# Performance work log

Hardware: AMD Instinct MI355X
Metric: run time of the kernel (lower is better)

The kernel has to match this reference:

```python
import jax, jax.numpy as jnp
import numpy as np

N_NODES = 1_000_000
N_EDGES = 8_000_000
EMB = 64
CHANNELS = 2
C_DIM = EMB // CHANNELS
NEG_SLOPE = 0.01  # nn.LeakyReLU default
EPS = 1e-10


def setup_inputs() -> dict:
    key = jax.random.key(0)
    k1, k2, k3, k4, k5 = jax.random.split(key, 5)
    ego_emb = jax.random.normal(k1, (N_NODES, EMB), dtype=jnp.float32)
    W = jax.random.normal(k2, (CHANNELS, EMB, C_DIM), dtype=jnp.float32) * (1.0 / np.sqrt(EMB))
    b = jax.random.normal(k3, (CHANNELS, 1, C_DIM), dtype=jnp.float32) * 0.01
    row_indices = jax.random.randint(k4, (N_EDGES,), 0, N_NODES, dtype=jnp.int32)
    col_indices = jax.random.randint(k5, (N_EDGES,), 0, N_NODES, dtype=jnp.int32)
    return {"ego_emb": ego_emb, "W": W, "b": b,
            "row_indices": row_indices, "col_indices": col_indices}


def _channel_gat(ego_emb, Wc, bc, row, col, n_nodes):
    # project nodes to this disentangled channel: [N, c_dim]
    h = jax.nn.leaky_relu(ego_emb @ Wc + bc, NEG_SLOPE)
    h_row = h[row]                      # [E, c_dim] edge gather (dst)
    h_col = h[col]                      # [E, c_dim] edge gather (src)
    logits = jax.nn.leaky_relu(jnp.sum(h_row * h_col, axis=-1), NEG_SLOPE)  # [E]
    # edge softmax per destination row (numerically stable)
    row_max = jax.ops.segment_max(logits, row, num_segments=n_nodes)
    ex = jnp.exp(logits - row_max[row])
    denom = jax.ops.segment_sum(ex, row, num_segments=n_nodes)
    alpha = ex / (denom[row] + EPS)     # [E]
    # scatter-add weighted messages into destination rows
    return jax.ops.segment_sum(alpha[:, None] * h_col, row, num_segments=n_nodes)


def reference(ego_emb, W, b, row_indices, col_indices):
    outs = [
        _channel_gat(ego_emb, W[c], b[c], row_indices, col_indices, ego_emb.shape[0])
        for c in range(CHANNELS)
    ]
    return jnp.concatenate(outs, axis=-1)  # [N, emb_size]
```

## Files before the change

kernel.cpp:

```cpp
#include <hip/hip_runtime.h>
#include <stdint.h>

#define NEG_SLOPE 0.01f
#define EPSF 1e-10f
#define NB_SHIFT 11
#define NB_ROWS (1 << NB_SHIFT)
#define NB_MAX 512
#define BP_EPT 16
#define BP_EDGES (256 * BP_EPT)
#define CB_CAP 20480

__device__ __forceinline__ float lrelu(float x){
  return fmaxf(x, 0.f) + NEG_SLOPE * fminf(x, 0.f);
}

__global__ void conv_wb(const float* __restrict__ W,
                        const float* __restrict__ b,
                        float* __restrict__ Wf, float* __restrict__ bf){
  int i = blockIdx.x * blockDim.x + threadIdx.x;
  for (int idx = i; idx < 64 * 64; idx += blockDim.x * gridDim.x){
    int k = idx >> 6, j = idx & 63;
    int c = j >> 5, jj = j & 31;
    Wf[idx] = W[c * 2048 + k * 32 + jj];
  }
  if (i < 64) bf[i] = b[i];
}

__global__ __launch_bounds__(256) void proj(const float* __restrict__ ego,
                                            const float* __restrict__ Wf,
                                            const float* __restrict__ bf,
                                            float* __restrict__ h, int N){
  int n = blockIdx.x * 256 + threadIdx.x;
  if (n >= N) return;
  float acc[64];
  #pragma unroll
  for (int j = 0; j < 64; j++) acc[j] = bf[j];
  const float4* ep = (const float4*)(ego + (size_t)n * 64);
  for (int kk = 0; kk < 16; kk++){
    float4 q = ep[kk];
    float ev[4] = {q.x, q.y, q.z, q.w};
    const float* wbase = Wf + kk * 4 * 64;
    #pragma unroll
    for (int t = 0; t < 4; t++){
      float ek = ev[t];
      const float* wrow = wbase + t * 64;
      #pragma unroll
      for (int j = 0; j < 64; j++) acc[j] = fmaf(ek, wrow[j], acc[j]);
    }
  }
  float4* hp = (float4*)(h + (size_t)n * 64);
  #pragma unroll
  for (int v = 0; v < 16; v++){
    float4 o;
    o.x = lrelu(acc[4 * v + 0]);
    o.y = lrelu(acc[4 * v + 1]);
    o.z = lrelu(acc[4 * v + 2]);
    o.w = lrelu(acc[4 * v + 3]);
    hp[v] = o;
  }
}

__global__ __launch_bounds__(256) void bhist(const int* __restrict__ row,
                                             int* __restrict__ bcnt, int E, int nb){
  __shared__ int lh[NB_MAX];
  for (int i = threadIdx.x; i < nb; i += 256) lh[i] = 0;
  __syncthreads();
  int i = blockIdx.x * 256 + threadIdx.x;
  int stride = gridDim.x * 256;
  for (; i < E; i += stride) atomicAdd(&lh[row[i] >> NB_SHIFT], 1);
  __syncthreads();
  for (int j = threadIdx.x; j < nb; j += 256){
    int v = lh[j];
    if (v) atomicAdd(&bcnt[j], v);
  }
}

__global__ __launch_bounds__(512) void bscan(const int* __restrict__ bcnt,
                                             int* __restrict__ bbase,
                                             int* __restrict__ bcur, int nb){
  __shared__ int sh[NB_MAX];
  int t = threadIdx.x;
  int v = (t < nb) ? bcnt[t] : 0;
  sh[t] = v; __syncthreads();
  for (int off = 1; off < NB_MAX; off <<= 1){
    int a = (t >= off) ? sh[t - off] : 0;
    __syncthreads();
    sh[t] += a;
    __syncthreads();
  }
  if (t < nb){
    int e = sh[t] - v;
    bbase[t] = e;
    bcur[t] = e;
  }
}

__global__ __launch_bounds__(256) void binpairs(const int* __restrict__ row,
                                                const int* __restrict__ col,
                                                int* __restrict__ bcur,
                                                unsigned int* __restrict__ tmp,
                                                int E, int nb){
  __shared__ int lh[NB_MAX];
  __shared__ int lofs[NB_MAX];
  __shared__ int lbase[NB_MAX];
  __shared__ int wsum[256];
  __shared__ unsigned int sval[BP_EDGES];
  __shared__ unsigned int sdst[BP_EDGES];
  int t = threadIdx.x;
  for (int i = t; i < nb; i += 256) lh[i] = 0;
  __syncthreads();
  int e0 = blockIdx.x * BP_EDGES;
  int tot = E - e0; if (tot > BP_EDGES) tot = BP_EDGES;
  int r[BP_EPT], c[BP_EPT], mo[BP_EPT];
  #pragma unroll
  for (int k = 0; k < BP_EPT; k++){
    int e = e0 + k * 256 + t;
    if (e < E){
      r[k] = row[e];
      c[k] = col[e];
      mo[k] = atomicAdd(&lh[r[k] >> NB_SHIFT], 1);
    } else r[k] = -1;
  }
  __syncthreads();
  int c0 = (2 * t < nb) ? lh[2 * t] : 0;
  int c1 = (2 * t + 1 < nb) ? lh[2 * t + 1] : 0;
  int s = c0 + c1;
  wsum[t] = s; __syncthreads();
  for (int off = 1; off < 256; off <<= 1){
    int a = (t >= off) ? wsum[t - off] : 0;
    __syncthreads();
    wsum[t] += a;
    __syncthreads();
  }
  int tb = wsum[t] - s;
  if (2 * t < nb){
    lofs[2 * t] = tb;
    if (c0) lbase[2 * t] = atomicAdd(&bcur[2 * t], c0);
  }
  if (2 * t + 1 < nb){
    lofs[2 * t + 1] = tb + c0;
    if (c1) lbase[2 * t + 1] = atomicAdd(&bcur[2 * t + 1], c1);
  }
  __syncthreads();
  #pragma unroll
  for (int k = 0; k < BP_EPT; k++){
    if (r[k] >= 0){
      int b = r[k] >> NB_SHIFT;
      int slot = lofs[b] + mo[k];
      sval[slot] = ((unsigned int)(r[k] & (NB_ROWS - 1)) << 20) | (unsigned int)c[k];
      sdst[slot] = (unsigned int)(lbase[b] + mo[k]);
    }
  }
  __syncthreads();
  for (int i = t; i < tot; i += 256) tmp[sdst[i]] = sval[i];
}

__global__ __launch_bounds__(512) void csrbuild(const unsigned int* __restrict__ tmp,
                                                const int* __restrict__ bbase,
                                                const int* __restrict__ bcnt,
                                                int* __restrict__ deg,
                                                int* __restrict__ offs,
                                                int* __restrict__ colp,
                                                int N){
  __shared__ int cnt[NB_ROWS];
  __shared__ int wsum[512];
  __shared__ int scol[CB_CAP];
  int b = blockIdx.x;
  int r0 = b << NB_SHIFT;
  int t = threadIdx.x;
  for (int i = t; i < NB_ROWS; i += 512) cnt[i] = 0;
  __syncthreads();
  int s = bbase[b];
  int cb = bcnt[b];
  int e = s + cb;
  for (int p = s + t; p < e; p += 512) atomicAdd(&cnt[tmp[p] >> 20], 1);
  __syncthreads();
  int base_i = t * 4;
  int dv[4], loc[4];
  int sum = 0;
  #pragma unroll
  for (int k = 0; k < 4; k++){
    dv[k] = cnt[base_i + k];
    loc[k] = sum;
    sum += dv[k];
  }
  wsum[t] = sum; __syncthreads();
  for (int off = 1; off < 512; off <<= 1){
    int a = (t >= off) ? wsum[t - off] : 0;
    __syncthreads();
    wsum[t] += a;
    __syncthreads();
  }
  int tbase = wsum[t] - sum;
  #pragma unroll
  for (int k = 0; k < 4; k++){
    int i = base_i + k;
    int o = tbase + loc[k];
    if (r0 + i < N){
      deg[r0 + i] = dv[k];
      offs[r0 + i] = s + o;
    }
    cnt[i] = o;
  }
  __syncthreads();
  if (cb <= CB_CAP){
    for (int p = s + t; p < e; p += 512){
      unsigned int v = tmp[p];
      int pos = atomicAdd(&cnt[v >> 20], 1);
      scol[pos] = (int)(v & 0xFFFFFu);
    }
    __syncthreads();
    for (int i = t; i < cb; i += 512) colp[s + i] = scol[i];
  } else {
    for (int p = s + t; p < e; p += 512){
      unsigned int v = tmp[p];
      int pos = atomicAdd(&cnt[v >> 20], 1);
      colp[s + pos] = (int)(v & 0xFFFFFu);
    }
  }
}

__global__ __launch_bounds__(256) void agg(const float* __restrict__ h,
                                           const int* __restrict__ offs,
                                           const int* __restrict__ deg,
                                           const int* __restrict__ colp,
                                           float* __restrict__ out, int N){
  int n = blockIdx.x * 256 + threadIdx.x;
  int ch = blockIdx.y;
  if (n >= N) return;
  const float4* hr4 = (const float4*)(h + (size_t)n * 64 + ch * 32);
  float hr[32];
  #pragma unroll
  for (int v = 0; v < 8; v++){
    float4 q = hr4[v];
    hr[4 * v + 0] = q.x; hr[4 * v + 1] = q.y; hr[4 * v + 2] = q.z; hr[4 * v + 3] = q.w;
  }
  float acc[32];
  #pragma unroll
  for (int j = 0; j < 32; j++) acc[j] = 0.f;
  float l = 0.f;
  int s = offs[n], d = deg[n];
  for (int p = s; p < s + d; ++p){
    int c = colp[p];
    const float4* hc4 = (const float4*)(h + (size_t)c * 64 + ch * 32);
    float hc[32];
    #pragma unroll
    for (int v = 0; v < 8; v++){
      float4 q = hc4[v];
      hc[4 * v + 0] = q.x; hc[4 * v + 1] = q.y; hc[4 * v + 2] = q.z; hc[4 * v + 3] = q.w;
    }
    float dot = 0.f;
    #pragma unroll
    for (int j = 0; j < 32; j++) dot = fmaf(hr[j], hc[j], dot);
    float lg = fminf(lrelu(dot), 80.f);
    float w = __expf(lg);
    l += w;
    #pragma unroll
    for (int j = 0; j < 32; j++) acc[j] = fmaf(w, hc[j], acc[j]);
  }
  float inv = 1.f / (l + EPSF);
  float4* op = (float4*)(out + (size_t)n * 64 + ch * 32);
  #pragma unroll
  for (int v = 0; v < 8; v++){
    float4 o;
    o.x = acc[4 * v + 0] * inv;
    o.y = acc[4 * v + 1] * inv;
    o.z = acc[4 * v + 2] * inv;
    o.w = acc[4 * v + 3] * inv;
    op[v] = o;
  }
}

extern "C" void kernel_launch(void* const* d_in, const int* in_sizes, int n_in,
                              void* d_out, int out_size, void* d_ws, size_t ws_size,
                              hipStream_t stream){
  const float* ego = (const float*)d_in[0];
  const float* W   = (const float*)d_in[1];
  const float* b   = (const float*)d_in[2];
  const int* row = (const int*)d_in[3];
  const int* col = (const int*)d_in[4];
  int N = in_sizes[0] / 64;
  int E = in_sizes[3];
  float* out = (float*)d_out;

  char* ws = (char*)d_ws;
  float* Wf = (float*)ws;
  float* bf = Wf + 4096;
  size_t off = 32768;
  float* h = (float*)(ws + off); off += (size_t)N * 64 * 4;
  int* deg  = (int*)(ws + off); off += (size_t)N * 4;
  int* offs = (int*)(ws + off); off += (size_t)N * 4;
  int* bcnt  = (int*)(ws + off); off += NB_MAX * 4;
  int* bbase = (int*)(ws + off); off += NB_MAX * 4;
  int* bcur  = (int*)(ws + off); off += NB_MAX * 4;
  unsigned int* tmp = (unsigned int*)(ws + off); off += (size_t)E * 4;
  int* colp = (int*)(ws + off);

  int nb = (N + NB_ROWS - 1) >> NB_SHIFT;

  hipMemsetAsync(bcnt, 0, NB_MAX * 4, stream);
  conv_wb<<<16, 256, 0, stream>>>(W, b, Wf, bf);
  proj<<<(N + 255) / 256, 256, 0, stream>>>(ego, Wf, bf, h, N);
  bhist<<<256, 256, 0, stream>>>(row, bcnt, E, nb);
  bscan<<<1, NB_MAX, 0, stream>>>(bcnt, bbase, bcur, nb);
  binpairs<<<(E + BP_EDGES - 1) / BP_EDGES, 256, 0, stream>>>(row, col, bcur, tmp, E, nb);
  csrbuild<<<nb, 512, 0, stream>>>(tmp, bbase, bcnt, deg, offs, colp, N);
  dim3 g((N + 255) / 256, 2);
  agg<<<g, 256, 0, stream>>>(h, offs, deg, colp, out, N);
}
```

Measured before the change: 1.274 ms.

## Store projected features in fp16 and fuse both channels into one aggregation pass

The projection now writes node features as packed half precision, which halves the bytes gathered per edge in aggregation. The aggregation kernel handles both channels in a single thread, so each edge reads its 128-byte neighbour row once and the column index once instead of twice. Offsets and degrees are packed into an int2, and the histogram grid is enlarged. The trade-offs are fp16 rounding error in the dot products and messages, and 64 float accumulators per thread, which raises register pressure and can lower occupancy.

```diff
diff --git a/kernel.cpp b/kernel.cpp
--- a/kernel.cpp
+++ b/kernel.cpp
@@ -1,4 +1,5 @@
 #include <hip/hip_runtime.h>
+#include <hip/hip_fp16.h>
 #include <stdint.h>
 
 #define NEG_SLOPE 0.01f
@@ -14,6 +15,15 @@
   return fmaxf(x, 0.f) + NEG_SLOPE * fminf(x, 0.f);
 }
 
+__device__ __forceinline__ unsigned pkh2(float a, float b){
+  __half2 h = __floats2half2_rn(a, b);
+  return __builtin_bit_cast(unsigned, h);
+}
+
+__device__ __forceinline__ float2 uph2(unsigned u){
+  return __half22float2(__builtin_bit_cast(__half2, u));
+}
+
 __global__ void conv_wb(const float* __restrict__ W,
                         const float* __restrict__ b,
                         float* __restrict__ Wf, float* __restrict__ bf){
@@ -29,7 +39,7 @@
 __global__ __launch_bounds__(256) void proj(const float* __restrict__ ego,
                                             const float* __restrict__ Wf,
                                             const float* __restrict__ bf,
-                                            float* __restrict__ h, int N){
+                                            __half* __restrict__ h2, int N){
   int n = blockIdx.x * 256 + threadIdx.x;
   if (n >= N) return;
   float acc[64];
@@ -48,15 +58,15 @@
       for (int j = 0; j < 64; j++) acc[j] = fmaf(ek, wrow[j], acc[j]);
     }
   }
-  float4* hp = (float4*)(h + (size_t)n * 64);
-  #pragma unroll
-  for (int v = 0; v < 16; v++){
-    float4 o;
-    o.x = lrelu(acc[4 * v + 0]);
-    o.y = lrelu(acc[4 * v + 1]);
-    o.z = lrelu(acc[4 * v + 2]);
-    o.w = lrelu(acc[4 * v + 3]);
-    hp[v] = o;
+  uint4* dst = (uint4*)(h2 + (size_t)n * 64);
+  #pragma unroll
+  for (int v = 0; v < 8; v++){
+    uint4 o;
+    o.x = pkh2(lrelu(acc[8 * v + 0]), lrelu(acc[8 * v + 1]));
+    o.y = pkh2(lrelu(acc[8 * v + 2]), lrelu(acc[8 * v + 3]));
+    o.z = pkh2(lrelu(acc[8 * v + 4]), lrelu(acc[8 * v + 5]));
+    o.w = pkh2(lrelu(acc[8 * v + 6]), lrelu(acc[8 * v + 7]));
+    dst[v] = o;
   }
 }
 
@@ -158,8 +168,7 @@
 __global__ __launch_bounds__(512) void csrbuild(const unsigned int* __restrict__ tmp,
                                                 const int* __restrict__ bbase,
                                                 const int* __restrict__ bcnt,
-                                                int* __restrict__ deg,
-                                                int* __restrict__ offs,
+                                                int2* __restrict__ odeg,
                                                 int* __restrict__ colp,
                                                 int N){
   __shared__ int cnt[NB_ROWS];
@@ -196,10 +205,7 @@
   for (int k = 0; k < 4; k++){
     int i = base_i + k;
     int o = tbase + loc[k];
-    if (r0 + i < N){
-      deg[r0 + i] = dv[k];
-      offs[r0 + i] = s + o;
-    }
+    if (r0 + i < N) odeg[r0 + i] = make_int2(s + o, dv[k]);
     cnt[i] = o;
   }
   __syncthreads();
@@ -220,53 +226,78 @@
   }
 }
 
-__global__ __launch_bounds__(256) void agg(const float* __restrict__ h,
-                                           const int* __restrict__ offs,
-                                           const int* __restrict__ deg,
-                                           const int* __restrict__ colp,
-                                           float* __restrict__ out, int N){
+__global__ __launch_bounds__(256) void agg2(const __half* __restrict__ h2,
+                                            const int2* __restrict__ odeg,
+                                            const int* __restrict__ colp,
+                                            float* __restrict__ out, int N){
   int n = blockIdx.x * 256 + threadIdx.x;
-  int ch = blockIdx.y;
   if (n >= N) return;
-  const float4* hr4 = (const float4*)(h + (size_t)n * 64 + ch * 32);
-  float hr[32];
+  unsigned hrp[32];
+  const uint4* hr4 = (const uint4*)(h2 + (size_t)n * 64);
   #pragma unroll
   for (int v = 0; v < 8; v++){
-    float4 q = hr4[v];
-    hr[4 * v + 0] = q.x; hr[4 * v + 1] = q.y; hr[4 * v + 2] = q.z; hr[4 * v + 3] = q.w;
-  }
-  float acc[32];
-  #pragma unroll
-  for (int j = 0; j < 32; j++) acc[j] = 0.f;
-  float l = 0.f;
-  int s = offs[n], d = deg[n];
+    uint4 q = hr4[v];
+    hrp[4 * v + 0] = q.x; hrp[4 * v + 1] = q.y;
+    hrp[4 * v + 2] = q.z; hrp[4 * v + 3] = q.w;
+  }
+  float acc[64];
+  #pragma unroll
+  for (int j = 0; j < 64; j++) acc[j] = 0.f;
+  float l0 = 0.f, l1 = 0.f;
+  int2 od = odeg[n];
+  int s = od.x, d = od.y;
   for (int p = s; p < s + d; ++p){
     int c = colp[p];
-    const float4* hc4 = (const float4*)(h + (size_t)c * 64 + ch * 32);
-    float hc[32];
+    unsigned hcp[32];
+    const uint4* hc4 = (const uint4*)(h2 + (size_t)c * 64);
     #pragma unroll
     for (int v = 0; v < 8; v++){
-      float4 q = hc4[v];
-      hc[4 * v + 0] = q.x; hc[4 * v + 1] = q.y; hc[4 * v + 2] = q.z; hc[4 * v + 3] = q.w;
-    }
-    float dot = 0.f;
-    #pragma unroll
-    for (int j = 0; j < 32; j++) dot = fmaf(hr[j], hc[j], dot);
-    float lg = fminf(lrelu(dot), 80.f);
-    float w = __expf(lg);
-    l += w;
-    #pragma unroll
-    for (int j = 0; j < 32; j++) acc[j] = fmaf(w, hc[j], acc[j]);
-  }
-  float inv = 1.f / (l + EPSF);
-  float4* op = (float4*)(out + (size_t)n * 64 + ch * 32);
-  #pragma unroll
-  for (int v = 0; v < 8; v++){
+      uint4 q = hc4[v];
+      hcp[4 * v + 0] = q.x; hcp[4 * v + 1] = q.y;
+      hcp[4 * v + 2] = q.z; hcp[4 * v + 3] = q.w;
+    }
+    float dot0 = 0.f, dot1 = 0.f;
+    #pragma unroll
+    for (int i = 0; i < 16; i++){
+      float2 a = uph2(hrp[i]);
+      float2 b = uph2(hcp[i]);
+      dot0 = fmaf(a.x, b.x, dot0);
+      dot0 = fmaf(a.y, b.y, dot0);
+    }
+    #pragma unroll
+    for (int i = 16; i < 32; i++){
+      float2 a = uph2(hrp[i]);
+      float2 b = uph2(hcp[i]);
+      dot1 = fmaf(a.x, b.x, dot1);
+      dot1 = fmaf(a.y, b.y, dot1);
+    }
+    float w0 = __expf(fminf(lrelu(dot0), 80.f));
+    float w1 = __expf(fminf(lrelu(dot1), 80.f));
+    l0 += w0; l1 += w1;
+    #pragma unroll
+    for (int i = 0; i < 16; i++){
+      float2 b = uph2(hcp[i]);
+      acc[2 * i + 0] = fmaf(w0, b.x, acc[2 * i + 0]);
+      acc[2 * i + 1] = fmaf(w0, b.y, acc[2 * i + 1]);
+    }
+    #pragma unroll
+    for (int i = 16; i < 32; i++){
+      float2 b = uph2(hcp[i]);
+      acc[2 * i + 0] = fmaf(w1, b.x, acc[2 * i + 0]);
+      acc[2 * i + 1] = fmaf(w1, b.y, acc[2 * i + 1]);
+    }
+  }
+  float inv0 = 1.f / (l0 + EPSF);
+  float inv1 = 1.f / (l1 + EPSF);
+  float4* op = (float4*)(out + (size_t)n * 64);
+  #pragma unroll
+  for (int v = 0; v < 16; v++){
+    float sc = (v < 8) ? inv0 : inv1;
     float4 o;
-    o.x = acc[4 * v + 0] * inv;
-    o.y = acc[4 * v + 1] * inv;
-    o.z = acc[4 * v + 2] * inv;
-    o.w = acc[4 * v + 3] * inv;
+    o.x = acc[4 * v + 0] * sc;
+    o.y = acc[4 * v + 1] * sc;
+    o.z = acc[4 * v + 2] * sc;
+    o.w = acc[4 * v + 3] * sc;
     op[v] = o;
   }
 }
@@ -287,9 +318,8 @@
   float* Wf = (float*)ws;
   float* bf = Wf + 4096;
   size_t off = 32768;
-  float* h = (float*)(ws + off); off += (size_t)N * 64 * 4;
-  int* deg  = (int*)(ws + off); off += (size_t)N * 4;
-  int* offs = (int*)(ws + off); off += (size_t)N * 4;
+  __half* h2 = (__half*)(ws + off); off += (size_t)N * 64 * 2;
+  int2* odeg = (int2*)(ws + off); off += (size_t)N * 8;
   int* bcnt  = (int*)(ws + off); off += NB_MAX * 4;
   int* bbase = (int*)(ws + off); off += NB_MAX * 4;
   int* bcur  = (int*)(ws + off); off += NB_MAX * 4;
@@ -300,11 +330,10 @@
 
   hipMemsetAsync(bcnt, 0, NB_MAX * 4, stream);
   conv_wb<<<16, 256, 0, stream>>>(W, b, Wf, bf);
-  proj<<<(N + 255) / 256, 256, 0, stream>>>(ego, Wf, bf, h, N);
-  bhist<<<256, 256, 0, stream>>>(row, bcnt, E, nb);
+  proj<<<(N + 255) / 256, 256, 0, stream>>>(ego, Wf, bf, h2, N);
+  bhist<<<1024, 256, 0, stream>>>(row, bcnt, E, nb);
   bscan<<<1, NB_MAX, 0, stream>>>(bcnt, bbase, bcur, nb);
   binpairs<<<(E + BP_EDGES - 1) / BP_EDGES, 256, 0, stream>>>(row, col, bcur, tmp, E, nb);
-  csrbuild<<<nb, 512, 0, stream>>>(tmp, bbase, bcnt, deg, offs, colp, N);
-  dim3 g((N + 255) / 256, 2);
-  agg<<<g, 256, 0, stream>>>(h, offs, deg, colp, out, N);
-}
+  csrbuild<<<nb, 512, 0, stream>>>(tmp, bbase, bcnt, odeg, colp, N);
+  agg2<<<(N + 255) / 256, 256, 0, stream>>>(h2, odeg, colp, out, N);
+}
```

Result: faster. 1.026 ms (-19.5%).
